# Kernel optimization log

Hardware: AMD Instinct MI355X
Metric: run time of the kernel (lower is better)

Reference implementation:

```python
import jax, jax.numpy as jnp
import numpy as np

D_MODEL = 512
NUM_HEADS = 8
HEAD_DIM = D_MODEL // NUM_HEADS  # 64


def setup_inputs() -> dict:
    key = jax.random.key(0)
    k_x, k_wqkv, k_bqkv, k_wout, k_bout = jax.random.split(key, 5)
    B, L = 30, 2048
    s_in = 1.0 / np.sqrt(D_MODEL)
    return {
        "x": jax.random.normal(k_x, (B, L, D_MODEL), dtype=jnp.float32),
        "w_qkv": jax.random.uniform(k_wqkv, (3 * D_MODEL, D_MODEL), minval=-s_in, maxval=s_in, dtype=jnp.float32),
        "b_qkv": jax.random.uniform(k_bqkv, (3 * D_MODEL,), minval=-s_in, maxval=s_in, dtype=jnp.float32),
        "w_out": jax.random.uniform(k_wout, (D_MODEL, D_MODEL), minval=-s_in, maxval=s_in, dtype=jnp.float32),
        "b_out": jax.random.uniform(k_bout, (D_MODEL,), minval=-s_in, maxval=s_in, dtype=jnp.float32),
    }


def reference(x, w_qkv, b_qkv, w_out, b_out):
    B, L, _ = x.shape
    # QKV projection: (B, L, 3*d_model)
    qkv = jnp.einsum("bld,ed->ble", x, w_qkv) + b_qkv
    # NOTE: source discards the permute, so layout stays (B, L, H, 3*head_dim)
    qkv = qkv.reshape(B, L, NUM_HEADS, 3 * HEAD_DIM)
    q, k, v = jnp.split(qkv, 3, axis=-1)  # each (B, L, H, head_dim)
    # Attention contracts head_dim -> (B, L, H, H): attention OVER HEADS, faithful to bug
    scores = jnp.einsum("blhd,blgd->blhg", q, k) / np.sqrt(HEAD_DIM)
    # mask=False in source adds 0 -> no-op
    attn = jax.nn.softmax(scores, axis=-1)
    val = jnp.einsum("blhg,blgd->blhd", attn, v).reshape(B, L, D_MODEL)
    out = jnp.einsum("bld,ed->ble", val, w_out) + b_out
    return out
```

## Files before the change

### kernel.cpp

```cpp
#include <hip/hip_runtime.h>
#include <hip/hip_bf16.h>
#include <stdint.h>

typedef short    s16x8  __attribute__((ext_vector_type(8)));
typedef __bf16   bf16x8 __attribute__((ext_vector_type(8)));
typedef float    f32x4  __attribute__((ext_vector_type(4)));

__device__ __forceinline__ unsigned short f2bf(float f) {
    union { float f; unsigned u; } v; v.f = f;
    unsigned r = v.u + 0x7FFFu + ((v.u >> 16) & 1u);
    return (unsigned short)(r >> 16);
}
__device__ __forceinline__ float bf2f(unsigned short s) {
    union { unsigned u; float f; } v; v.u = ((unsigned)s) << 16;
    return v.f;
}

__device__ __forceinline__ void gload16(const void* g, void* l) {
    __builtin_amdgcn_global_load_lds(
        (const __attribute__((address_space(1))) void*)(uintptr_t)g,
        (__attribute__((address_space(3))) void*)(uintptr_t)l,
        16, 0, 0);
}

__global__ __launch_bounds__(256) void cvt_bf16(const float* __restrict__ in,
                                                unsigned short* __restrict__ out,
                                                int n4) {
    int i = blockIdx.x * blockDim.x + threadIdx.x;
    int stride = gridDim.x * blockDim.x;
    for (; i < n4; i += stride) {
        const float4 v = *(const float4*)(in + (size_t)i * 4);
        ushort4 o;
        o.x = f2bf(v.x); o.y = f2bf(v.y); o.z = f2bf(v.z); o.w = f2bf(v.w);
        *(ushort4*)(out + (size_t)i * 4) = o;
    }
}

template<int K, bool OUT_BF16>
__global__ __launch_bounds__(256, 2) void gemm128(
        const unsigned short* __restrict__ A,
        const unsigned short* __restrict__ B,
        const float* __restrict__ bias,
        void* __restrict__ Cvoid,
        int M, int N, int ntn) {
    constexpr int BM = 128, BN = 128, BK = 64, NT = K / BK;
    __shared__ __align__(16) unsigned short As[2][BM * BK];
    __shared__ __align__(16) unsigned short Bs[2][BN * BK];
    const int tid  = threadIdx.x;
    const int lane = tid & 63;
    const int wv   = tid >> 6;
    const int nwg  = (int)gridDim.x;
    const int wg   = ((int)blockIdx.x & 7) * (nwg >> 3) + ((int)blockIdx.x >> 3);
    const int bm   = wg / ntn;
    const int bn   = wg % ntn;
    const int wr   = (wv >> 1) * 64;
    const int wc   = (wv & 1) * 64;
    const int lr   = lane & 15;
    const int ls   = lane >> 4;

    const unsigned short* Ag = A + (size_t)bm * BM * K;
    const unsigned short* Bg = B + (size_t)bn * BN * K;

    auto stage = [&](int t) {
        char* la = (char*)As[t & 1];
        char* lb = (char*)Bs[t & 1];
        #pragma unroll
        for (int p = 0; p < 4; ++p) {
            const int c     = p * 256 + tid;
            const int row   = c >> 3;
            const int slot  = c & 7;
            const int gslot = slot ^ (row & 7);
            gload16(Ag + (size_t)row * K + t * BK + gslot * 8, la + c * 16);
            gload16(Bg + (size_t)row * K + t * BK + gslot * 8, lb + c * 16);
        }
    };
    auto frag = [&](const unsigned short* lds, int row, int ks) -> bf16x8 {
        const int slot = ks ^ (row & 7);
        return *(const bf16x8*)((const char*)lds + row * (BK * 2) + slot * 16);
    };

    f32x4 acc[4][4] = {};

    stage(0);

    #pragma unroll
    for (int t = 0; t < NT; ++t) {
        asm volatile("s_waitcnt vmcnt(0)" ::: "memory");
        __syncthreads();
        if (t + 1 < NT) stage(t + 1);

        bf16x8 af[2][4], bf[2][4];
        #pragma unroll
        for (int h = 0; h < 2; ++h) {
            #pragma unroll
            for (int m = 0; m < 4; ++m)
                af[h][m] = frag(As[t & 1], wr + m * 16 + lr, h * 4 + ls);
            #pragma unroll
            for (int n = 0; n < 4; ++n)
                bf[h][n] = frag(Bs[t & 1], wc + n * 16 + lr, h * 4 + ls);
        }

        __builtin_amdgcn_s_setprio(1);
        #pragma unroll
        for (int h = 0; h < 2; ++h)
            #pragma unroll
            for (int m = 0; m < 4; ++m)
                #pragma unroll
                for (int n = 0; n < 4; ++n)
                    acc[m][n] = __builtin_amdgcn_mfma_f32_16x16x32_bf16(
                        af[h][m], bf[h][n], acc[m][n], 0, 0, 0);
        __builtin_amdgcn_s_setprio(0);
    }

    const int r0 = bm * BM + wr + ls * 4;
    const int c0 = bn * BN + wc + lr;
    #pragma unroll
    for (int n = 0; n < 4; ++n) {
        const int gc = c0 + n * 16;
        const float bv = bias[gc];
        #pragma unroll
        for (int m = 0; m < 4; ++m) {
            #pragma unroll
            for (int j = 0; j < 4; ++j) {
                const int gr = r0 + m * 16 + j;
                const float v = acc[m][n][j] + bv;
                if constexpr (OUT_BF16)
                    ((unsigned short*)Cvoid)[(size_t)gr * N + gc] = f2bf(v);
                else
                    ((float*)Cvoid)[(size_t)gr * N + gc] = v;
            }
        }
    }
}

__global__ __launch_bounds__(256) void attn_heads(
        const unsigned short* __restrict__ qkv,
        unsigned short* __restrict__ val,
        int M) {
    const int t    = blockIdx.x * 4 + (threadIdx.x >> 6);
    const int lane = threadIdx.x & 63;
    const int h    = lane >> 3;
    const int c    = lane & 7;
    const unsigned short* base = qkv + (size_t)t * 1536;

    s16x8 q8 = *(const s16x8*)(base + h * 192 + c * 8);
    float qf[8];
    #pragma unroll
    for (int j = 0; j < 8; ++j) qf[j] = bf2f((unsigned short)q8[j]);

    float s[8];
    #pragma unroll
    for (int g = 0; g < 8; ++g) {
        s16x8 k8 = *(const s16x8*)(base + g * 192 + 64 + c * 8);
        float p = 0.f;
        #pragma unroll
        for (int j = 0; j < 8; ++j) p += qf[j] * bf2f((unsigned short)k8[j]);
        s[g] = p;
    }
    #pragma unroll
    for (int mask = 1; mask <= 4; mask <<= 1)
        #pragma unroll
        for (int g = 0; g < 8; ++g)
            s[g] += __shfl_xor(s[g], mask, 64);

    float mx = -1e30f;
    #pragma unroll
    for (int g = 0; g < 8; ++g) { s[g] *= 0.125f; mx = fmaxf(mx, s[g]); }
    float sum = 0.f;
    #pragma unroll
    for (int g = 0; g < 8; ++g) { s[g] = __expf(s[g] - mx); sum += s[g]; }
    const float inv = 1.f / sum;

    float acc[8] = {0.f,0.f,0.f,0.f,0.f,0.f,0.f,0.f};
    #pragma unroll
    for (int g = 0; g < 8; ++g) {
        s16x8 v8 = *(const s16x8*)(base + g * 192 + 128 + c * 8);
        const float ag = s[g] * inv;
        #pragma unroll
        for (int j = 0; j < 8; ++j) acc[j] += ag * bf2f((unsigned short)v8[j]);
    }
    s16x8 ov;
    #pragma unroll
    for (int j = 0; j < 8; ++j) ov[j] = (short)f2bf(acc[j]);
    *(s16x8*)(val + (size_t)t * 512 + h * 64 + c * 8) = ov;
}

extern "C" void kernel_launch(void* const* d_in, const int* in_sizes, int n_in,
                              void* d_out, int out_size, void* d_ws, size_t ws_size,
                              hipStream_t stream) {
    const float* x     = (const float*)d_in[0];
    const float* w_qkv = (const float*)d_in[1];
    const float* b_qkv = (const float*)d_in[2];
    const float* w_out = (const float*)d_in[3];
    const float* b_out = (const float*)d_in[4];
    float* out = (float*)d_out;

    const int DM = 512;
    const int M  = in_sizes[0] / DM;

    unsigned short* xb    = (unsigned short*)d_ws;
    unsigned short* wqkvb = xb + (size_t)M * DM;
    unsigned short* woutb = wqkvb + (size_t)3 * DM * DM;
    unsigned short* qkvb  = woutb + (size_t)DM * DM;
    unsigned short* valb  = xb;

    cvt_bf16<<<2048, 256, 0, stream>>>(x, xb, M * DM / 4);
    cvt_bf16<<<96,   256, 0, stream>>>(w_qkv, wqkvb, 3 * DM * DM / 4);
    cvt_bf16<<<32,   256, 0, stream>>>(w_out, woutb, DM * DM / 4);

    gemm128<512, true><<<dim3((M / 128) * (3 * DM / 128)), 256, 0, stream>>>(
        xb, wqkvb, b_qkv, qkvb, M, 3 * DM, 3 * DM / 128);

    attn_heads<<<M / 4, 256, 0, stream>>>(qkvb, valb, M);

    gemm128<512, false><<<dim3((M / 128) * (DM / 128)), 256, 0, stream>>>(
        valb, woutb, b_out, out, M, DM, DM / 128);
}
```

Measured before the change: 256.9 us.

## Fuse fp32-to-bf16 conversion of x into QKV GEMM with resident A tile

Drops the separate x conversion kernel and its bf16 round trip through memory. The QKV projection now loads a 64-row fp32 strip of x, converts it to bf16 straight into swizzled LDS, and keeps it resident while streaming all twelve 128-column weight chunks through a double buffer. Each block then makes only one pass over x, but tiles are smaller (64x128 per block), so there is less MFMA work per weight load and fewer blocks (M/64). The initial x load is not overlapped with compute, and 64KB of resident LDS may limit occupancy.

```diff
diff --git a/kernel.cpp b/kernel.cpp
--- a/kernel.cpp
+++ b/kernel.cpp
@@ -33,6 +33,116 @@
         ushort4 o;
         o.x = f2bf(v.x); o.y = f2bf(v.y); o.z = f2bf(v.z); o.w = f2bf(v.w);
         *(ushort4*)(out + (size_t)i * 4) = o;
+    }
+}
+
+template<int K>
+__global__ __launch_bounds__(256, 2) void gemm1_fused(
+        const float* __restrict__ X,
+        const unsigned short* __restrict__ W,
+        const float* __restrict__ bias,
+        unsigned short* __restrict__ Q,
+        int M, int N) {
+    constexpr int TM = 64, CN = 128, BK = 32;
+    constexpr int NT = K / BK;
+    constexpr int NW = 12 * NT;
+    __shared__ __align__(16) unsigned short Asm[TM * K];
+    __shared__ __align__(16) unsigned short Bsm[2][CN * BK];
+    const int tid  = threadIdx.x;
+    const int lane = tid & 63;
+    const int wv   = tid >> 6;
+    const int nwg  = (int)gridDim.x;
+    const int bm   = ((int)blockIdx.x & 7) * (nwg >> 3) + ((int)blockIdx.x >> 3);
+    const int wr   = (wv >> 1) * 32;
+    const int wc   = (wv & 1) * 64;
+    const int lr   = lane & 15;
+    const int ls   = lane >> 4;
+
+    {
+        const float* xb = X + (size_t)bm * TM * K;
+        #pragma unroll
+        for (int i = 0; i < 16; ++i) {
+            const int g    = i * 256 + tid;
+            const int row  = g >> 6;
+            const int slot = g & 63;
+            const float4 v0 = *(const float4*)(xb + (size_t)g * 8);
+            const float4 v1 = *(const float4*)(xb + (size_t)g * 8 + 4);
+            s16x8 o;
+            o[0] = (short)f2bf(v0.x); o[1] = (short)f2bf(v0.y);
+            o[2] = (short)f2bf(v0.z); o[3] = (short)f2bf(v0.w);
+            o[4] = (short)f2bf(v1.x); o[5] = (short)f2bf(v1.y);
+            o[6] = (short)f2bf(v1.z); o[7] = (short)f2bf(v1.w);
+            const int phys = slot ^ (row & 7);
+            *(s16x8*)((char*)Asm + row * (K * 2) + phys * 16) = o;
+        }
+    }
+
+    auto stageB = [&](int w) {
+        const int nc = w >> 4, t = w & 15;
+        char* lb = (char*)Bsm[w & 1];
+        const int c     = tid;
+        #pragma unroll
+        for (int p = 0; p < 2; ++p) {
+            const int cc    = p * 256 + c;
+            const int row   = cc >> 2;
+            const int slot  = cc & 3;
+            const int gslot = slot ^ ((row >> 1) & 3);
+            gload16(W + (size_t)(nc * CN + row) * K + t * BK + gslot * 8,
+                    lb + cc * 16);
+        }
+    };
+    auto fragB = [&](int w, int row) -> bf16x8 {
+        const int slot = ls ^ ((row >> 1) & 3);
+        return *(const bf16x8*)((const char*)Bsm[w & 1] + row * (BK * 2) + slot * 16);
+    };
+    auto fragA = [&](int t, int row) -> bf16x8 {
+        const int slot = (t * 4 + ls) ^ (row & 7);
+        return *(const bf16x8*)((const char*)Asm + row * (K * 2) + slot * 16);
+    };
+
+    f32x4 acc[2][4] = {};
+
+    stageB(0);
+
+    for (int w = 0; w < NW; ++w) {
+        const int t = w & 15, nc = w >> 4;
+        asm volatile("s_waitcnt vmcnt(0)" ::: "memory");
+        __syncthreads();
+        if (w + 1 < NW) stageB(w + 1);
+
+        bf16x8 af[2], bf[4];
+        #pragma unroll
+        for (int m = 0; m < 2; ++m) af[m] = fragA(t, wr + m * 16 + lr);
+        #pragma unroll
+        for (int n = 0; n < 4; ++n) bf[n] = fragB(w, wc + n * 16 + lr);
+
+        __builtin_amdgcn_s_setprio(1);
+        #pragma unroll
+        for (int m = 0; m < 2; ++m)
+            #pragma unroll
+            for (int n = 0; n < 4; ++n)
+                acc[m][n] = __builtin_amdgcn_mfma_f32_16x16x32_bf16(
+                    af[m], bf[n], acc[m][n], 0, 0, 0);
+        __builtin_amdgcn_s_setprio(0);
+
+        if (t == 15) {
+            const int r0 = bm * TM + wr + ls * 4;
+            const int c0 = nc * CN + wc + lr;
+            #pragma unroll
+            for (int n = 0; n < 4; ++n) {
+                const int gc = c0 + n * 16;
+                const float bv = bias[gc];
+                #pragma unroll
+                for (int m = 0; m < 2; ++m) {
+                    #pragma unroll
+                    for (int j = 0; j < 4; ++j) {
+                        Q[(size_t)(r0 + m * 16 + j) * N + gc] =
+                            f2bf(acc[m][n][j] + bv);
+                        acc[m][n][j] = 0.f;
+                    }
+                }
+            }
+        }
     }
 }
 
@@ -198,18 +308,16 @@
     const int DM = 512;
     const int M  = in_sizes[0] / DM;
 
-    unsigned short* xb    = (unsigned short*)d_ws;
-    unsigned short* wqkvb = xb + (size_t)M * DM;
+    unsigned short* wqkvb = (unsigned short*)d_ws;
     unsigned short* woutb = wqkvb + (size_t)3 * DM * DM;
     unsigned short* qkvb  = woutb + (size_t)DM * DM;
-    unsigned short* valb  = xb;
-
-    cvt_bf16<<<2048, 256, 0, stream>>>(x, xb, M * DM / 4);
-    cvt_bf16<<<96,   256, 0, stream>>>(w_qkv, wqkvb, 3 * DM * DM / 4);
-    cvt_bf16<<<32,   256, 0, stream>>>(w_out, woutb, DM * DM / 4);
-
-    gemm128<512, true><<<dim3((M / 128) * (3 * DM / 128)), 256, 0, stream>>>(
-        xb, wqkvb, b_qkv, qkvb, M, 3 * DM, 3 * DM / 128);
+    unsigned short* valb  = qkvb + (size_t)M * 3 * DM;
+
+    cvt_bf16<<<96, 256, 0, stream>>>(w_qkv, wqkvb, 3 * DM * DM / 4);
+    cvt_bf16<<<32, 256, 0, stream>>>(w_out, woutb, DM * DM / 4);
+
+    gemm1_fused<512><<<dim3(M / 64), 256, 0, stream>>>(
+        x, wqkvb, b_qkv, qkvb, M, 3 * DM);
 
     attn_heads<<<M / 4, 256, 0, stream>>>(qkvb, valb, M);
 
```

Result: slower. 313.9 us (+22.2%).

## Fuse fp32-to-bf16 conversion of x into the QKV GEMM A-tile staging

Applied to the files above, without the earlier changes.

Removes the separate cvt_bf16 pass over x. The QKV GEMM now reads fp32 activations directly, converts them to bf16 in registers and writes them into swizzled LDS. This saves a full read and write of the large activation tensor, and valb moves to its own workspace slot. In exchange, the A tile is loaded synchronously through registers instead of asynchronously with global_load_lds, which can stall the prefetch before the MFMA work. Each block also reads twice as many A bytes.

```diff
diff --git a/kernel.cpp b/kernel.cpp
--- a/kernel.cpp
+++ b/kernel.cpp
@@ -33,6 +33,116 @@
         ushort4 o;
         o.x = f2bf(v.x); o.y = f2bf(v.y); o.z = f2bf(v.z); o.w = f2bf(v.w);
         *(ushort4*)(out + (size_t)i * 4) = o;
+    }
+}
+
+template<int K>
+__global__ __launch_bounds__(256, 2) void gemm1f(
+        const float* __restrict__ X,
+        const unsigned short* __restrict__ B,
+        const float* __restrict__ bias,
+        unsigned short* __restrict__ C,
+        int M, int N, int ntn) {
+    constexpr int BM = 128, BN = 128, BK = 64, NT = K / BK;
+    __shared__ __align__(16) unsigned short As[2][BM * BK];
+    __shared__ __align__(16) unsigned short Bs[2][BN * BK];
+    const int tid  = threadIdx.x;
+    const int lane = tid & 63;
+    const int wv   = tid >> 6;
+    const int nwg  = (int)gridDim.x;
+    const int wg   = ((int)blockIdx.x & 7) * (nwg >> 3) + ((int)blockIdx.x >> 3);
+    const int bm   = wg / ntn;
+    const int bn   = wg % ntn;
+    const int wr   = (wv >> 1) * 64;
+    const int wc   = (wv & 1) * 64;
+    const int lr   = lane & 15;
+    const int ls   = lane >> 4;
+
+    const float*          Ag = X + (size_t)bm * BM * K;
+    const unsigned short* Bg = B + (size_t)bn * BN * K;
+
+    auto stageA = [&](int t) {
+        char* la = (char*)As[t & 1];
+        #pragma unroll
+        for (int p = 0; p < 4; ++p) {
+            const int c     = p * 256 + tid;
+            const int row   = c >> 3;
+            const int slot  = c & 7;
+            const int gslot = slot ^ (row & 7);
+            const float* src = Ag + (size_t)row * K + t * BK + gslot * 8;
+            const float4 v0 = *(const float4*)(src);
+            const float4 v1 = *(const float4*)(src + 4);
+            s16x8 o;
+            o[0] = (short)f2bf(v0.x); o[1] = (short)f2bf(v0.y);
+            o[2] = (short)f2bf(v0.z); o[3] = (short)f2bf(v0.w);
+            o[4] = (short)f2bf(v1.x); o[5] = (short)f2bf(v1.y);
+            o[6] = (short)f2bf(v1.z); o[7] = (short)f2bf(v1.w);
+            *(s16x8*)(la + c * 16) = o;
+        }
+    };
+    auto stageB = [&](int t) {
+        char* lb = (char*)Bs[t & 1];
+        #pragma unroll
+        for (int p = 0; p < 4; ++p) {
+            const int c     = p * 256 + tid;
+            const int row   = c >> 3;
+            const int slot  = c & 7;
+            const int gslot = slot ^ (row & 7);
+            gload16(Bg + (size_t)row * K + t * BK + gslot * 8, lb + c * 16);
+        }
+    };
+    auto frag = [&](const unsigned short* lds, int row, int ks) -> bf16x8 {
+        const int slot = ks ^ (row & 7);
+        return *(const bf16x8*)((const char*)lds + row * (BK * 2) + slot * 16);
+    };
+
+    f32x4 acc[4][4] = {};
+
+    stageB(0); stageA(0);
+
+    #pragma unroll
+    for (int t = 0; t < NT; ++t) {
+        asm volatile("s_waitcnt vmcnt(0)" ::: "memory");
+        __syncthreads();
+        if (t + 1 < NT) { stageB(t + 1); stageA(t + 1); }
+
+        bf16x8 af[2][4], bf[2][4];
+        #pragma unroll
+        for (int h = 0; h < 2; ++h) {
+            #pragma unroll
+            for (int m = 0; m < 4; ++m)
+                af[h][m] = frag(As[t & 1], wr + m * 16 + lr, h * 4 + ls);
+            #pragma unroll
+            for (int n = 0; n < 4; ++n)
+                bf[h][n] = frag(Bs[t & 1], wc + n * 16 + lr, h * 4 + ls);
+        }
+
+        __builtin_amdgcn_s_setprio(1);
+        #pragma unroll
+        for (int h = 0; h < 2; ++h)
+            #pragma unroll
+            for (int m = 0; m < 4; ++m)
+                #pragma unroll
+                for (int n = 0; n < 4; ++n)
+                    acc[m][n] = __builtin_amdgcn_mfma_f32_16x16x32_bf16(
+                        af[h][m], bf[h][n], acc[m][n], 0, 0, 0);
+        __builtin_amdgcn_s_setprio(0);
+    }
+
+    const int r0 = bm * BM + wr + ls * 4;
+    const int c0 = bn * BN + wc + lr;
+    #pragma unroll
+    for (int n = 0; n < 4; ++n) {
+        const int gc = c0 + n * 16;
+        const float bv = bias[gc];
+        #pragma unroll
+        for (int m = 0; m < 4; ++m) {
+            #pragma unroll
+            for (int j = 0; j < 4; ++j) {
+                const int gr = r0 + m * 16 + j;
+                C[(size_t)gr * N + gc] = f2bf(acc[m][n][j] + bv);
+            }
+        }
     }
 }
 
@@ -198,18 +308,16 @@
     const int DM = 512;
     const int M  = in_sizes[0] / DM;
 
-    unsigned short* xb    = (unsigned short*)d_ws;
-    unsigned short* wqkvb = xb + (size_t)M * DM;
+    unsigned short* wqkvb = (unsigned short*)d_ws;
     unsigned short* woutb = wqkvb + (size_t)3 * DM * DM;
     unsigned short* qkvb  = woutb + (size_t)DM * DM;
-    unsigned short* valb  = xb;
-
-    cvt_bf16<<<2048, 256, 0, stream>>>(x, xb, M * DM / 4);
-    cvt_bf16<<<96,   256, 0, stream>>>(w_qkv, wqkvb, 3 * DM * DM / 4);
-    cvt_bf16<<<32,   256, 0, stream>>>(w_out, woutb, DM * DM / 4);
-
-    gemm128<512, true><<<dim3((M / 128) * (3 * DM / 128)), 256, 0, stream>>>(
-        xb, wqkvb, b_qkv, qkvb, M, 3 * DM, 3 * DM / 128);
+    unsigned short* valb  = qkvb + (size_t)M * 3 * DM;
+
+    cvt_bf16<<<96, 256, 0, stream>>>(w_qkv, wqkvb, 3 * DM * DM / 4);
+    cvt_bf16<<<32, 256, 0, stream>>>(w_out, woutb, DM * DM / 4);
+
+    gemm1f<512><<<dim3((M / 128) * (3 * DM / 128)), 256, 0, stream>>>(
+        x, wqkvb, b_qkv, qkvb, M, 3 * DM, 3 * DM / 128);
 
     attn_heads<<<M / 4, 256, 0, stream>>>(qkvb, valb, M);
 
```

Measured after the change: 331.5 us. +29.1%, slower.
